# Kernel optimization log

Measured on AMD Instinct MI355X. Metric: run time of the kernel, lower is better.

Reference implementation:

```python
import jax, jax.numpy as jnp
import numpy as np

B, S, HID = 1, 2048, 2048
NH, NKV, HD = 32, 8, 64  # query heads, kv heads, head dim
NEG = -1e9


def rotate_half(x):
    d = x.shape[-1] // 2
    return jnp.concatenate([-x[..., d:], x[..., :d]], axis=-1)


def setup_inputs() -> dict:
    key = jax.random.key(0)
    ks = jax.random.split(key, 8)
    hidden_states = jax.random.normal(ks[0], (B, S, HID), dtype=jnp.float32)
    # RoPE angles: realistic cos/sin tables (B, S, HD)
    inv_freq = 1.0 / (10000.0 ** (np.arange(0, HD, 2, dtype=np.float32) / HD))
    pos = np.arange(S, dtype=np.float32)
    ang = pos[:, None] * inv_freq[None, :]            # (S, HD/2)
    ang = np.concatenate([ang, ang], axis=-1)          # (S, HD)
    cos = jnp.broadcast_to(jnp.cos(ang)[None], (B, S, HD)).astype(jnp.float32)
    sin = jnp.broadcast_to(jnp.sin(ang)[None], (B, S, HD)).astype(jnp.float32)
    # additive causal mask (B, 1, S, S)
    causal = jnp.where(jnp.tril(jnp.ones((S, S), dtype=bool)), 0.0, NEG).astype(jnp.float32)
    attention_mask = jnp.broadcast_to(causal[None, None], (B, 1, S, S))
    std = 0.02
    Wq = jax.random.normal(ks[1], (NH * HD, HID), dtype=jnp.float32) * std
    Wk = jax.random.normal(ks[2], (NKV * HD, HID), dtype=jnp.float32) * std
    Wv = jax.random.normal(ks[3], (NKV * HD, HID), dtype=jnp.float32) * std
    Wo = jax.random.normal(ks[4], (HID, NH * HD), dtype=jnp.float32) * std
    return {"hidden_states": hidden_states, "cos": cos, "sin": sin,
            "attention_mask": attention_mask, "Wq": Wq, "Wk": Wk, "Wv": Wv, "Wo": Wo}


def reference(hidden_states, cos, sin, attention_mask, Wq, Wk, Wv, Wo):
    scaling = HD ** -0.5
    n_rep = NH // NKV
    # projections -> (B, H, S, D)
    q = jnp.einsum('bsh,qh->bsq', hidden_states, Wq).reshape(B, S, NH, HD).transpose(0, 2, 1, 3)
    k = jnp.einsum('bsh,qh->bsq', hidden_states, Wk).reshape(B, S, NKV, HD).transpose(0, 2, 1, 3)
    v = jnp.einsum('bsh,qh->bsq', hidden_states, Wv).reshape(B, S, NKV, HD).transpose(0, 2, 1, 3)
    # RoPE (cos/sin broadcast over head dim via [:, None])
    c, s = cos[:, None], sin[:, None]
    q = q * c + rotate_half(q) * s
    k = k * c + rotate_half(k) * s
    # GQA repeat_kv
    k = jnp.repeat(k, n_rep, axis=1)
    v = jnp.repeat(v, n_rep, axis=1)
    # eager attention
    attn_weights = jnp.einsum('bhqd,bhkd->bhqk', q, k) * scaling
    attn_weights = attn_weights + attention_mask
    attn_weights = jax.nn.softmax(attn_weights.astype(jnp.float32), axis=-1).astype(q.dtype)
    attn_output = jnp.einsum('bhqk,bhkd->bhqd', attn_weights, v)
    attn_output = attn_output.transpose(0, 2, 1, 3).reshape(B, S, NH * HD)
    attn_output = jnp.einsum('bsq,hq->bsh', attn_output, Wo)
    return attn_output, attn_weights
```

## Files before the change

kernel.cpp:

```cpp
#include <hip/hip_runtime.h>

#define S_LEN 2048
#define NH 32
#define NKV 8
#define HD 64
#define QH_DIM (NH * HD)
#define QKV_DIM 3072
#define K_OFF 2048
#define V_OFF 2560
#define LOG2E 1.44269504089f

typedef __attribute__((ext_vector_type(8))) __bf16 bf16x8;
typedef __attribute__((ext_vector_type(4))) float fx4;
typedef __attribute__((ext_vector_type(8))) unsigned short ush8;

__device__ __forceinline__ unsigned short f2bf(float f) {
  return __builtin_bit_cast(unsigned short, (__bf16)f);
}
__device__ __forceinline__ float bf2f(unsigned short h) {
  unsigned int u = ((unsigned int)h) << 16;
  return __builtin_bit_cast(float, u);
}
__device__ __forceinline__ fx4 zero4() {
  fx4 z; z[0] = 0.f; z[1] = 0.f; z[2] = 0.f; z[3] = 0.f; return z;
}

#define MFMA16(a, b, c) __builtin_amdgcn_mfma_f32_16x16x32_bf16((a), (b), (c), 0, 0, 0)

__device__ __forceinline__ void gl16(const void* g, void* l) {
  __builtin_amdgcn_global_load_lds((const __attribute__((address_space(1))) void*)g,
                                   (__attribute__((address_space(3))) void*)l, 16, 0, 0);
}

__global__ __launch_bounds__(256) void cast5(const float* __restrict__ s0, unsigned short* d0, int n0,
                                             const float* __restrict__ s1, unsigned short* d1, int n1,
                                             const float* __restrict__ s2, unsigned short* d2, int n2,
                                             const float* __restrict__ s3, unsigned short* d3, int n3,
                                             const float* __restrict__ s4, unsigned short* d4, int n4) {
  int i = blockIdx.x * 256 + threadIdx.x;
  const float* s;
  unsigned short* d;
  if (i < n0) { s = s0; d = d0; }
  else if ((i -= n0) < n1) { s = s1; d = d1; }
  else if ((i -= n1) < n2) { s = s2; d = d2; }
  else if ((i -= n2) < n3) { s = s3; d = d3; }
  else if ((i -= n3) < n4) { s = s4; d = d4; }
  else return;
  float4 v = ((const float4*)s)[i];
  ushort4 o;
  o.x = f2bf(v.x); o.y = f2bf(v.y); o.z = f2bf(v.z); o.w = f2bf(v.w);
  ((ushort4*)d)[i] = o;
}

__global__ __launch_bounds__(512, 6) void gemm_split(const unsigned short* __restrict__ A,
                                                     const unsigned short* __restrict__ B,
                                                     unsigned short* __restrict__ Part,
                                                     int M, int N, int K, int KH) {
  __shared__ unsigned short As[2][128 * 32];
  __shared__ unsigned short Bs[2][128 * 32];
  const int tid = threadIdx.x;
  const int bn = blockIdx.x * 128, bm = blockIdx.y * 128;
  const int kslice = blockIdx.z;
  const size_t koff = (size_t)kslice * KH;
  const int lane = tid & 63, wid = tid >> 6;
  const int lo = lane & 15, g = lane >> 4;
  const int wr = wid >> 2, wc = wid & 3;

  fx4 acc[4][2];
#pragma unroll
  for (int i = 0; i < 4; i++)
#pragma unroll
    for (int j = 0; j < 2; j++) acc[i][j] = zero4();

  const int srow = tid >> 2;
  const int cg = (tid & 3) ^ ((srow >> 1) & 3);
  const unsigned short* apg = &A[(size_t)(bm + srow) * K + koff + cg * 8];
  const unsigned short* bpg = &B[(size_t)(bn + srow) * K + koff + cg * 8];

  const int arow = wr * 64 + lo;
  const int brow = wc * 32 + lo;
  const int sc = (g ^ ((lo >> 1) & 3)) * 8;

#define G_STAGE(s, k0)                  \
  do {                                  \
    gl16(apg + (k0), &As[s][tid * 8]);  \
    gl16(bpg + (k0), &Bs[s][tid * 8]);  \
  } while (0)

#define G_COMPUTE(s)                                                   \
  do {                                                                 \
    bf16x8 af[4], bb[2];                                               \
    _Pragma("unroll") for (int mi = 0; mi < 4; mi++)                   \
        af[mi] = *(const bf16x8*)&As[s][(arow + mi * 16) * 32 + sc];   \
    _Pragma("unroll") for (int nj = 0; nj < 2; nj++)                   \
        bb[nj] = *(const bf16x8*)&Bs[s][(brow + nj * 16) * 32 + sc];   \
    _Pragma("unroll") for (int mi = 0; mi < 4; mi++)                   \
        _Pragma("unroll") for (int nj = 0; nj < 2; nj++)               \
            acc[mi][nj] = MFMA16(af[mi], bb[nj], acc[mi][nj]);         \
  } while (0)

  const int NT = KH >> 5;
  G_STAGE(0, 0);
  __syncthreads();
  int cur = 0;
  for (int t = 0; t < NT - 1; ++t) {
    G_STAGE(cur ^ 1, (t + 1) * 32);
    G_COMPUTE(cur);
    __syncthreads();
    cur ^= 1;
  }
  G_COMPUTE(cur);
#undef G_STAGE
#undef G_COMPUTE

  unsigned short* const pb = &Part[(size_t)kslice * M * N];
#pragma unroll
  for (int mi = 0; mi < 4; mi++)
#pragma unroll
    for (int nj = 0; nj < 2; nj++)
#pragma unroll
      for (int r = 0; r < 4; r++) {
        int row = bm + wr * 64 + mi * 16 + g * 4 + r;
        int col = bn + wc * 32 + nj * 16 + lo;
        pb[(size_t)row * N + col] = f2bf(acc[mi][nj][r]);
      }
}

__global__ __launch_bounds__(256) void combine_qkv(const unsigned short* __restrict__ P0,
                                                   const unsigned short* __restrict__ P1,
                                                   unsigned short* __restrict__ qkv,
                                                   const float* __restrict__ cosp,
                                                   const float* __restrict__ sinp,
                                                   unsigned short* __restrict__ Vt) {
  __shared__ unsigned short t[64][72];
  const int b = blockIdx.x;
  if (b < 2560) {
    int idx = b * 256 + threadIdx.x;
    int j = idx & 7;
    int tt = idx >> 3;
    int head = tt % 40;
    int s = tt / 40;
    const float scale = (head < 32) ? 0.125f * LOG2E : 1.0f;
    const size_t base = (size_t)s * QKV_DIM + head * 64 + j * 4;
    ushort4 a0l = *(const ushort4*)&P0[base];
    ushort4 a1l = *(const ushort4*)&P1[base];
    ushort4 a0h = *(const ushort4*)&P0[base + 32];
    ushort4 a1h = *(const ushort4*)&P1[base + 32];
    float xl0 = bf2f(a0l.x) + bf2f(a1l.x), xl1 = bf2f(a0l.y) + bf2f(a1l.y);
    float xl2 = bf2f(a0l.z) + bf2f(a1l.z), xl3 = bf2f(a0l.w) + bf2f(a1l.w);
    float xh0 = bf2f(a0h.x) + bf2f(a1h.x), xh1 = bf2f(a0h.y) + bf2f(a1h.y);
    float xh2 = bf2f(a0h.z) + bf2f(a1h.z), xh3 = bf2f(a0h.w) + bf2f(a1h.w);
    fx4 cl = *(const fx4*)&cosp[s * 64 + j * 4];
    fx4 ch = *(const fx4*)&cosp[s * 64 + 32 + j * 4];
    fx4 sl = *(const fx4*)&sinp[s * 64 + j * 4];
    fx4 sh = *(const fx4*)&sinp[s * 64 + 32 + j * 4];
    ushort4 ol, oh;
    ol.x = f2bf((xl0 * cl[0] - xh0 * sl[0]) * scale);
    ol.y = f2bf((xl1 * cl[1] - xh1 * sl[1]) * scale);
    ol.z = f2bf((xl2 * cl[2] - xh2 * sl[2]) * scale);
    ol.w = f2bf((xl3 * cl[3] - xh3 * sl[3]) * scale);
    oh.x = f2bf((xh0 * ch[0] + xl0 * sh[0]) * scale);
    oh.y = f2bf((xh1 * ch[1] + xl1 * sh[1]) * scale);
    oh.z = f2bf((xh2 * ch[2] + xl2 * sh[2]) * scale);
    oh.w = f2bf((xh3 * ch[3] + xl3 * sh[3]) * scale);
    *(ushort4*)&qkv[base] = ol;
    *(ushort4*)&qkv[base + 32] = oh;
  } else {
    const int tid = threadIdx.x;
    const int bb = b - 2560;
    const int cb = (bb & 7) * 64;
    const int rb = (bb >> 3) * 64;
#pragma unroll
    for (int rr = 0; rr < 2; rr++) {
      int row = rr * 32 + (tid >> 3);
      int c8 = (tid & 7) * 8;
      const size_t src = (size_t)(rb + row) * QKV_DIM + V_OFF + cb + c8;
      ush8 a = *(const ush8*)&P0[src];
      ush8 c = *(const ush8*)&P1[src];
      ush8 o;
#pragma unroll
      for (int j = 0; j < 8; j++) o[j] = f2bf(bf2f(a[j]) + bf2f(c[j]));
      *(ush8*)&t[row][c8] = o;
    }
    __syncthreads();
#pragma unroll
    for (int rr = 0; rr < 2; rr++) {
      int col = rr * 32 + (tid >> 3);
      int r8 = (tid & 7) * 8;
      ush8 o;
#pragma unroll
      for (int j = 0; j < 8; j++) o[j] = t[r8 + j][col];
      *(ush8*)&Vt[(size_t)(cb + col) * S_LEN + rb + r8] = o;
    }
  }
}

__global__ __launch_bounds__(256) void combine_wo(const unsigned short* __restrict__ P0,
                                                  const unsigned short* __restrict__ P1,
                                                  float* __restrict__ out) {
  const int i = blockIdx.x * 256 + threadIdx.x;
  const size_t base = (size_t)i * 8;
  ush8 a = *(const ush8*)&P0[base];
  ush8 b = *(const ush8*)&P1[base];
  fx4 o0, o1;
#pragma unroll
  for (int j = 0; j < 4; j++) o0[j] = bf2f(a[j]) + bf2f(b[j]);
#pragma unroll
  for (int j = 0; j < 4; j++) o1[j] = bf2f(a[4 + j]) + bf2f(b[4 + j]);
  *(fx4*)&out[base] = o0;
  *(fx4*)&out[base + 4] = o1;
}

__global__ __launch_bounds__(512, 4) void attn_kernel(const unsigned short* __restrict__ Q,
                                                      const unsigned short* __restrict__ Kb,
                                                      const unsigned short* __restrict__ Vt,
                                                      float* __restrict__ P,
                                                      unsigned short* __restrict__ AO) {
  __shared__ __align__(16) unsigned short pls[16][2048];
  __shared__ float lred[8][16];
  const int h = blockIdx.x;
  const int rt = 127 - blockIdx.y;
  const int hkv = h >> 2;
  const int wid = threadIdx.x >> 6, lane = threadIdx.x & 63;
  const int lo = lane & 15, g = lane >> 4;
  const int rowb = rt * 16;
  const int nkt = (rt + 4) >> 2;
  const int qg = rowb + lo;
  char* const plsb = (char*)pls;
  const int swz = (lo & 7) << 4;

  {
    const int zc0 = nkt * 64;
    const int nz4 = (S_LEN - zc0) >> 2;
    for (int idx = threadIdx.x; idx < 16 * nz4; idx += 512) {
      const int r = idx / nz4;
      const int c = idx - r * nz4;
      __builtin_nontemporal_store(zero4(),
          (fx4*)&P[((size_t)h * S_LEN + rowb + r) * S_LEN + zc0 + c * 4]);
    }
  }

  const bf16x8 qa0 = *(const bf16x8*)&Q[(size_t)qg * QKV_DIM + h * HD + g * 8];
  const bf16x8 qa1 = *(const bf16x8*)&Q[(size_t)qg * QKV_DIM + h * HD + 32 + g * 8];

  float l = 0.f;
  fx4 oacc[4];
#pragma unroll
  for (int dj = 0; dj < 4; dj++) oacc[dj] = zero4();

  {
    bf16x8 kc0[4], kc1[4];
    if (wid < nkt) {
#pragma unroll
      for (int nj = 0; nj < 4; nj++) {
        const int kcol = wid * 64 + nj * 16 + lo;
        kc0[nj] = *(const bf16x8*)&Kb[(size_t)kcol * QKV_DIM + hkv * HD + g * 8];
        kc1[nj] = *(const bf16x8*)&Kb[(size_t)kcol * QKV_DIM + hkv * HD + 32 + g * 8];
      }
    }
    for (int kt = wid; kt < nkt; kt += 8) {
      bf16x8 kn0[4], kn1[4];
      if (kt + 8 < nkt) {
#pragma unroll
        for (int nj = 0; nj < 4; nj++) {
          const int kcol = (kt + 8) * 64 + nj * 16 + lo;
          kn0[nj] = *(const bf16x8*)&Kb[(size_t)kcol * QKV_DIM + hkv * HD + g * 8];
          kn1[nj] = *(const bf16x8*)&Kb[(size_t)kcol * QKV_DIM + hkv * HD + 32 + g * 8];
        }
      }
      fx4 acc[4];
      __builtin_amdgcn_s_setprio(1);
#pragma unroll
      for (int nj = 0; nj < 4; nj++) {
        acc[nj] = MFMA16(kc0[nj], qa0, zero4());
        acc[nj] = MFMA16(kc1[nj], qa1, acc[nj]);
      }
      __builtin_amdgcn_s_setprio(0);
      const bool diag = (kt == nkt - 1);
#pragma unroll
      for (int nj = 0; nj < 4; nj++) {
        float e[4];
#pragma unroll
        for (int r = 0; r < 4; r++) {
          float v = exp2f(acc[nj][r]);
          if (diag && (kt * 64 + nj * 16 + g * 4 + r > qg)) v = 0.f;
          l += v;
          e[r] = v;
        }
        unsigned int w0 = (unsigned int)f2bf(e[0]) | ((unsigned int)f2bf(e[1]) << 16);
        unsigned int w1 = (unsigned int)f2bf(e[2]) | ((unsigned int)f2bf(e[3]) << 16);
        uint2 w; w.x = w0; w.y = w1;
        *(uint2*)(plsb + lo * 4096 + ((kt * 128 + nj * 32 + g * 8) ^ swz)) = w;
      }
#pragma unroll
      for (int kk = 0; kk < 2; kk++) {
        bf16x8 pa = *(const bf16x8*)(plsb + lo * 4096 + ((kt * 128 + kk * 64 + g * 16) ^ swz));
        __builtin_amdgcn_s_setprio(1);
#pragma unroll
        for (int dj = 0; dj < 4; dj++) {
          bf16x8 vb = *(const bf16x8*)&Vt[(size_t)(hkv * HD + dj * 16 + lo) * S_LEN +
                                          kt * 64 + kk * 32 + g * 8];
          oacc[dj] = MFMA16(pa, vb, oacc[dj]);
        }
        __builtin_amdgcn_s_setprio(0);
      }
#pragma unroll
      for (int j = 0; j < 4; j++) { kc0[j] = kn0[j]; kc1[j] = kn1[j]; }
    }
  }
  l += __shfl_xor(l, 16);
  l += __shfl_xor(l, 32);
  if (lane < 16) lred[wid][lo] = l;

  __syncthreads();

  float pinv[4];
#pragma unroll
  for (int it = 0; it < 4; it++) {
    const int rho = it * 4 + g;
    pinv[it] = 1.f / (lred[0][rho] + lred[1][rho] + lred[2][rho] + lred[3][rho] +
                      lred[4][rho] + lred[5][rho] + lred[6][rho] + lred[7][rho]);
  }
  float* const pbase = &P[((size_t)h * S_LEN + rowb) * S_LEN];

  for (int kt = wid; kt < nkt; kt += 8) {
#pragma unroll
    for (int it = 0; it < 4; it++) {
      const int rho = it * 4 + g;
      ushort4 b4 = *(const ushort4*)(plsb + rho * 4096 +
                                     ((kt * 128 + lo * 8) ^ ((rho & 7) << 4)));
      fx4 pv;
      pv[0] = bf2f(b4.x) * pinv[it]; pv[1] = bf2f(b4.y) * pinv[it];
      pv[2] = bf2f(b4.z) * pinv[it]; pv[3] = bf2f(b4.w) * pinv[it];
      __builtin_nontemporal_store(pv,
          (fx4*)&pbase[(size_t)rho * S_LEN + kt * 64 + lo * 4]);
    }
  }

  __syncthreads();
  fx4* const obp = (fx4*)plsb;
#pragma unroll
  for (int dj = 0; dj < 4; dj++) obp[wid * 256 + dj * 64 + lane] = oacc[dj];
  __syncthreads();
  if (wid < 4) {
    fx4 s = obp[wid * 64 + lane];
#pragma unroll
    for (int ww = 1; ww < 8; ww++) {
      fx4 t2 = obp[ww * 256 + wid * 64 + lane];
#pragma unroll
      for (int j = 0; j < 4; j++) s[j] += t2[j];
    }
#pragma unroll
    for (int r = 0; r < 4; r++) {
      const int q = g * 4 + r;
      const float linv = 1.f / (lred[0][q] + lred[1][q] + lred[2][q] + lred[3][q] +
                                lred[4][q] + lred[5][q] + lred[6][q] + lred[7][q]);
      AO[(size_t)(rowb + q) * QH_DIM + h * HD + wid * 16 + lo] = f2bf(s[r] * linv);
    }
  }
}

extern "C" void kernel_launch(void* const* d_in, const int* in_sizes, int n_in,
                              void* d_out, int out_size, void* d_ws, size_t ws_size,
                              hipStream_t stream) {
  const float* hs = (const float*)d_in[0];
  const float* cosp = (const float*)d_in[1];
  const float* sinp = (const float*)d_in[2];
  const float* Wq = (const float*)d_in[4];
  const float* Wk = (const float*)d_in[5];
  const float* Wv = (const float*)d_in[6];
  const float* Wo = (const float*)d_in[7];

  char* w = (char*)d_ws;
  unsigned short* wo_bf   = (unsigned short*)(w);
  unsigned short* ao_bf   = (unsigned short*)(w + (((size_t)9) << 20));
  unsigned short* hs_bf   = (unsigned short*)(w + (((size_t)18) << 20));
  unsigned short* wqkv_bf = (unsigned short*)(w + (((size_t)27) << 20));
  unsigned short* qkv_bf  = (unsigned short*)(w + (((size_t)40) << 20));
  unsigned short* vt_bf   = (unsigned short*)(w + (((size_t)53) << 20));
  unsigned short* wop     = hs_bf;

  float* out0 = (float*)d_out;
  float* P = out0 + (size_t)S_LEN * QH_DIM;
  const size_t P_BYTES = (size_t)NH * S_LEN * S_LEN * 4;
  const size_t QKVP_BYTES = (size_t)2 * S_LEN * QKV_DIM * 2;
  unsigned short* qkvp = (unsigned short*)((char*)P + P_BYTES - QKVP_BYTES);

  cast5<<<14336, 256, 0, stream>>>(hs, hs_bf, 1048576,
                                   Wq, wqkv_bf, 1048576,
                                   Wk, wqkv_bf + (size_t)K_OFF * 2048, 262144,
                                   Wv, wqkv_bf + (size_t)V_OFF * 2048, 262144,
                                   Wo, wo_bf, 1048576);

  gemm_split<<<dim3(QKV_DIM / 128, 16, 2), 512, 0, stream>>>(hs_bf, wqkv_bf, qkvp,
                                                             2048, QKV_DIM, 2048, 1024);

  combine_qkv<<<2816, 256, 0, stream>>>(qkvp, qkvp + (size_t)S_LEN * QKV_DIM,
                                        qkv_bf, cosp, sinp, vt_bf);

  attn_kernel<<<dim3(NH, 128), 512, 0, stream>>>(qkv_bf, qkv_bf + K_OFF, vt_bf, P, ao_bf);

  gemm_split<<<dim3(16, 16, 2), 512, 0, stream>>>(ao_bf, wo_bf, wop, 2048, 2048, 2048, 1024);

  combine_wo<<<2048, 256, 0, stream>>>(wop, wop + (size_t)S_LEN * QH_DIM, out0);
}
```

Baseline: 254.0 us.

## Move causal zero-fill of attention weights into projection GEMM main loops

The upper-triangle zero stores for the attention-probability output are removed from the attention kernel. They are now spread across the K-loop iterations of the two split-K GEMMs. The QKV GEMM zeroes heads 0-23, and the output-projection GEMM zeroes heads 24-31, because the QKV partials are parked in the tail of that buffer until attention has consumed them. The aim is to overlap this large write stream with GEMM compute and shorten the attention kernel. The total bytes written stay the same, and the GEMMs pick up extra store traffic and index arithmetic.

After: 258.9 us. Within noise of the previous version (+2.0%).

```diff
diff --git a/kernel.cpp b/kernel.cpp
--- a/kernel.cpp
+++ b/kernel.cpp
@@ -55,7 +55,8 @@
 __global__ __launch_bounds__(512, 6) void gemm_split(const unsigned short* __restrict__ A,
                                                      const unsigned short* __restrict__ B,
                                                      unsigned short* __restrict__ Part,
-                                                     int M, int N, int K, int KH) {
+                                                     int M, int N, int K, int KH,
+                                                     float* __restrict__ Zp, int zmode) {
   __shared__ unsigned short As[2][128 * 32];
   __shared__ unsigned short Bs[2][128 * 32];
   const int tid = threadIdx.x;
@@ -80,6 +81,18 @@
   const int arow = wr * 64 + lo;
   const int brow = wc * 32 + lo;
   const int sc = (g ^ ((lo >> 1) & 3)) * 8;
+
+  const int bid2 = blockIdx.y * gridDim.x + blockIdx.x;
+  int zhead, zpair, zbase, zn;
+  if (zmode == 0) {
+    zhead = bid2 >> 4; zpair = bid2 & 15;
+    zbase = blockIdx.z * 15872; zn = 31;
+  } else {
+    zhead = 24 + (bid2 >> 5); zpair = (bid2 >> 1) & 15;
+    zbase = (((bid2 & 1) << 1) | blockIdx.z) * 7936; zn = 16;
+  }
+  const int SA = (31 - zpair) << 10;
+  float* const zP = Zp + (size_t)zhead * S_LEN * S_LEN;
 
 #define G_STAGE(s, k0)                  \
   do {                                  \
@@ -104,6 +117,14 @@
   __syncthreads();
   int cur = 0;
   for (int t = 0; t < NT - 1; ++t) {
+    if (t < zn && !(zmode == 1 && t == 15 && tid >= 256)) {
+      int j = zbase + t * 512 + tid;
+      int b, jj;
+      if (j < SA) { b = zpair; jj = j; } else { b = 31 - zpair; jj = j - SA; }
+      const int row = (b << 6) + ((jj >> 4) & 63);
+      const int col4 = ((b + 1) << 4) + ((jj >> 10) << 4) + (jj & 15);
+      __builtin_nontemporal_store(zero4(), (fx4*)&zP[((size_t)row << 11) + (col4 << 2)]);
+    }
     G_STAGE(cur ^ 1, (t + 1) * 32);
     G_COMPUTE(cur);
     __syncthreads();
@@ -229,17 +250,6 @@
   char* const plsb = (char*)pls;
   const int swz = (lo & 7) << 4;
 
-  {
-    const int zc0 = nkt * 64;
-    const int nz4 = (S_LEN - zc0) >> 2;
-    for (int idx = threadIdx.x; idx < 16 * nz4; idx += 512) {
-      const int r = idx / nz4;
-      const int c = idx - r * nz4;
-      __builtin_nontemporal_store(zero4(),
-          (fx4*)&P[((size_t)h * S_LEN + rowb + r) * S_LEN + zc0 + c * 4]);
-    }
-  }
-
   const bf16x8 qa0 = *(const bf16x8*)&Q[(size_t)qg * QKV_DIM + h * HD + g * 8];
   const bf16x8 qa1 = *(const bf16x8*)&Q[(size_t)qg * QKV_DIM + h * HD + 32 + g * 8];
 
@@ -393,14 +403,17 @@
                                    Wo, wo_bf, 1048576);
 
   gemm_split<<<dim3(QKV_DIM / 128, 16, 2), 512, 0, stream>>>(hs_bf, wqkv_bf, qkvp,
-                                                             2048, QKV_DIM, 2048, 1024);
+                                                             2048, QKV_DIM, 2048, 1024,
+                                                             P, 0);
 
   combine_qkv<<<2816, 256, 0, stream>>>(qkvp, qkvp + (size_t)S_LEN * QKV_DIM,
                                         qkv_bf, cosp, sinp, vt_bf);
 
   attn_kernel<<<dim3(NH, 128), 512, 0, stream>>>(qkv_bf, qkv_bf + K_OFF, vt_bf, P, ao_bf);
 
-  gemm_split<<<dim3(16, 16, 2), 512, 0, stream>>>(ao_bf, wo_bf, wop, 2048, 2048, 2048, 1024);
+  gemm_split<<<dim3(16, 16, 2), 512, 0, stream>>>(ao_bf, wo_bf, wop,
+                                                  2048, 2048, 2048, 1024,
+                                                  P, 1);
 
   combine_wo<<<2048, 256, 0, stream>>>(wop, wop + (size_t)S_LEN * QH_DIM, out0);
 }
```
